# Kernel optimization log

Hardware: AMD Instinct MI355X
Metric: run time of the kernel (lower is better)

Reference implementation:

```python
import jax, jax.numpy as jnp
import numpy as np

B, S, D, E, TOPK, H = 8, 2048, 2048, 8, 2, 16
DH = D // H          # head_dim = 128
FH = D // H          # head_hidden_dim = 128 (hidden == dim, forced by linear3 shapes)
ROUTE_LEN = 2048     # x0 = x[:, :2048]


def setup_inputs() -> dict:
    key = jax.random.key(0)
    ks = jax.random.split(key, 8)
    s = 0.02
    return {
        "x": jax.random.normal(ks[0], (B, S, D), jnp.float32),
        "switch_w": jax.random.normal(ks[1], (E, D * ROUTE_LEN), jnp.float32) * s,
        "switch_b": jnp.zeros((E,), jnp.float32),
        "w1": jax.random.normal(ks[2], (E, FH, DH), jnp.float32) * s,
        "b1": jnp.zeros((E, FH), jnp.float32),
        "w2": jax.random.normal(ks[3], (E, DH, FH), jnp.float32) * s,
        "b2": jnp.zeros((E, DH), jnp.float32),
        "w3": jax.random.normal(ks[4], (D, D), jnp.float32) * s,
        "b3": jnp.zeros((D,), jnp.float32),
    }


def reference(x, switch_w, switch_b, w1, b1, w2, b2, w3, b3):
    b, s, d = x.shape
    # --- router: per batch-sample softmax over experts, top-k selection ---
    x0 = x[:, :ROUTE_LEN].reshape(b, -1)                      # [B, 2048*D]
    logits = x0 @ switch_w.T + switch_b                       # [B, E]
    probs = jax.nn.softmax(logits, axis=-1)
    gate, top_idx = jax.lax.top_k(probs, TOPK)                # [B, K]
    # --- split heads ---
    xh = x.reshape(b, s, H, DH).transpose(0, 2, 1, 3)         # [B, H, S, Dh]
    # --- per-sample gather of selected expert weights (dense grouped GEMM) ---
    w1s, b1s = w1[top_idx], b1[top_idx]                       # [B,K,F,Dh], [B,K,F]
    w2s, b2s = w2[top_idx], b2[top_idx]                       # [B,K,Dh,F], [B,K,Dh]
    h = jnp.einsum('bhsd,bkfd->bkhsf', xh, w1s) + b1s[:, :, None, None, :]
    h = jax.nn.gelu(h, approximate=False)                     # torch nn.GELU is exact
    o = jnp.einsum('bkhsf,bkdf->bkhsd', h, w2s) + b2s[:, :, None, None, :]
    # gate-weighted combine over selected experts (index_add_ sums the k copies)
    o = (o * gate[:, :, None, None, None]).sum(axis=1)        # [B, H, S, Dh]
    o = o.transpose(0, 2, 1, 3).reshape(b, s, d)              # combine heads
    out = x + o                                               # residual
    return out @ w3.T + b3                                    # linear3
```

## Files before the change

kernel.cpp:

```cpp
#include <hip/hip_runtime.h>
#include <math.h>

typedef unsigned short u16;
typedef unsigned int u32;
typedef __attribute__((ext_vector_type(8))) short short8;
typedef __attribute__((ext_vector_type(4))) float f32x4;
typedef __attribute__((ext_vector_type(4))) unsigned short ushort4v;

#define B_ 8
#define S_ 2048
#define D_ 2048
#define H_ 16
#define RLEN 4194304
#define NCHUNK 512

static __device__ __forceinline__ u16 f2bf(float f) {
    union { float f; u32 u; } v; v.f = f;
    u32 r = v.u + 0x7fffu + ((v.u >> 16) & 1u);
    return (u16)(r >> 16);
}
static __device__ __forceinline__ float bf2f(u16 u) {
    union { u32 u; float f; } v; v.u = ((u32)u) << 16;
    return v.f;
}
static __device__ __forceinline__ float gelu_fast(float v) {
    float z = 1.5957691216057308f * v * (1.0f + 0.044715f * v * v);
    float e = __expf(z);
    float r = __builtin_amdgcn_rcpf(e + 1.0f);
    return v * (1.0f - r);
}
static __device__ __forceinline__ f32x4 ntload4(const float* p) {
    return __builtin_nontemporal_load((const f32x4*)p);
}

typedef const __attribute__((address_space(1))) u32* gas1_t;
typedef __attribute__((address_space(3))) u32* las3_t;
static __device__ __forceinline__ void gload_lds16(const void* g, void* l) {
    __builtin_amdgcn_global_load_lds((gas1_t)g, (las3_t)l, 16, 0, 0);
}

template<int XB>
__global__ __launch_bounds__(256, 3) void router_partial(const float* __restrict__ x,
                                                         const float* __restrict__ sw,
                                                         float* __restrict__ part,
                                                         u16* __restrict__ xb) {
    int c = blockIdx.x;
    int t = threadIdx.x;
    const int chunk = RLEN / NCHUNK;
    int base = c * chunk;
    float acc[8][8];
#pragma unroll
    for (int b = 0; b < 8; b++)
#pragma unroll
        for (int e = 0; e < 8; e++) acc[b][e] = 0.f;

    for (int it = 0; it < chunk / (256 * 4); ++it) {
        int i = base + (it * 256 + t) * 4;
        f32x4 xv[8];
#pragma unroll
        for (int b = 0; b < 8; b++) xv[b] = ntload4(&x[(size_t)b * RLEN + i]);
        if (XB) {
            int row = i >> 7, col = i & 127;
            int scol = (((col >> 3) ^ (row & 7)) << 3) | (col & 7);
#pragma unroll
            for (int b = 0; b < 8; b++) {
                ushort4v u;
                u.x = f2bf(xv[b].x); u.y = f2bf(xv[b].y);
                u.z = f2bf(xv[b].z); u.w = f2bf(xv[b].w);
                *(ushort4v*)&xb[(size_t)b * RLEN + (size_t)row * 128 + scol] = u;
            }
        }
        f32x4 sv = ntload4(&sw[i]);
#pragma unroll
        for (int e = 0; e < 8; e++) {
            f32x4 svn;
            if (e < 7) svn = ntload4(&sw[(size_t)(e + 1) * RLEN + i]);
#pragma unroll
            for (int b = 0; b < 8; b++)
                acc[b][e] += xv[b].x * sv.x + xv[b].y * sv.y +
                             xv[b].z * sv.z + xv[b].w * sv.w;
            sv = svn;
        }
    }

    __shared__ float red[4][64];
    int lane = t & 63, wv = t >> 6;
#pragma unroll
    for (int q = 0; q < 64; q++) {
        float v = acc[q >> 3][q & 7];
#pragma unroll
        for (int m = 32; m >= 1; m >>= 1) v += __shfl_xor(v, m, 64);
        if (lane == 0) red[wv][q] = v;
    }
    __syncthreads();
    if (t < 64) {
        float s = red[0][t] + red[1][t] + red[2][t] + red[3][t];
        part[(size_t)t * NCHUNK + c] = s;
    }
}

__global__ __launch_bounds__(512) void router_finish(const float* __restrict__ part,
                                                     const float* __restrict__ swb,
                                                     const float* __restrict__ b2,
                                                     float* __restrict__ gate,
                                                     int* __restrict__ idx,
                                                     float* __restrict__ bc) {
    int t = threadIdx.x;
    __shared__ float lg[64];
    __shared__ float sg[16];
    __shared__ int   si[16];
    {
        int row = t >> 3, seg = t & 7;
        const float* p = part + (size_t)row * NCHUNK + seg * 64;
        float s = 0.f;
#pragma unroll 8
        for (int c = 0; c < 64; c++) s += p[c];
#pragma unroll
        for (int m = 4; m >= 1; m >>= 1) s += __shfl_down(s, m, 64);
        if (seg == 0) lg[row] = s + swb[row & 7];
    }
    __syncthreads();
    if (t < 8) {
        int b = t;
        float m = -1e30f;
        for (int e = 0; e < 8; e++) m = fmaxf(m, lg[b * 8 + e]);
        float p[8]; float sum = 0.f;
        for (int e = 0; e < 8; e++) { p[e] = expf(lg[b * 8 + e] - m); sum += p[e]; }
        for (int e = 0; e < 8; e++) p[e] /= sum;
        int i1 = 0; float v1 = p[0];
        for (int e = 1; e < 8; e++) if (p[e] > v1) { v1 = p[e]; i1 = e; }
        int i2 = -1; float v2 = -1.f;
        for (int e = 0; e < 8; e++) if (e != i1 && p[e] > v2) { v2 = p[e]; i2 = e; }
        gate[b * 2 + 0] = v1; gate[b * 2 + 1] = v2;
        idx[b * 2 + 0] = i1;  idx[b * 2 + 1] = i2;
        sg[b * 2] = v1; sg[b * 2 + 1] = v2;
        si[b * 2] = i1; si[b * 2 + 1] = i2;
    }
    __syncthreads();
    if (t < 128)
        for (int b = 0; b < 8; b++)
            bc[b * 128 + t] = sg[b * 2] * b2[si[b * 2] * 128 + t] +
                              sg[b * 2 + 1] * b2[si[b * 2 + 1] * 128 + t];
}

__global__ __launch_bounds__(256) void convert_w12(const float* __restrict__ w1,
                                                   const float* __restrict__ w2,
                                                   u16* __restrict__ w1b,
                                                   u16* __restrict__ w2b) {
    int i4 = (blockIdx.x * 256 + threadIdx.x) * 4;
    if (i4 < 131072) {
        int k = i4 & 127, f = (i4 >> 7) & 127;
        float4 v = *(const float4*)&w1[i4];
        int sc = ((((k >> 3) ^ (f & 7)) << 3) | (k & 7));
        ushort4v u;
        u.x = f2bf(v.x); u.y = f2bf(v.y); u.z = f2bf(v.z); u.w = f2bf(v.w);
        *(ushort4v*)&w1b[(i4 & ~127) + sc] = u;
    } else {
        int j = i4 - 131072;
        float4 v = *(const float4*)&w2[j];
        ushort4v u;
        u.x = f2bf(v.x); u.y = f2bf(v.y); u.z = f2bf(v.z); u.w = f2bf(v.w);
        *(ushort4v*)&w2b[j] = u;
    }
}

__global__ __launch_bounds__(256) void convert_w3(const float* __restrict__ w3,
                                                  u16* __restrict__ w3b) {
    size_t i = ((size_t)blockIdx.x * 256 + threadIdx.x) * 4;
    float4 v = *(const float4*)&w3[i];
    u16* d = &w3b[i];
    d[0] = f2bf(v.x); d[1] = f2bf(v.y); d[2] = f2bf(v.z); d[3] = f2bf(v.w);
}

template<int XB>
__global__ __launch_bounds__(512) void mlp_kernel(const void* __restrict__ xsrc_,
                                                  const u16* __restrict__ w1b,
                                                  const u16* __restrict__ w2b,
                                                  const float* __restrict__ b1,
                                                  const float* __restrict__ gate,
                                                  const int* __restrict__ idx,
                                                  const float* __restrict__ bc,
                                                  u16* __restrict__ y) {
    __shared__ __align__(16) u16 w1s[256 * 128];
    __shared__ __align__(16) u16 xs[2][64 * 128];
    __shared__ __align__(16) u16 hb[2][32 * 256];
    __shared__ __align__(16) u16 ob[2][32 * 128];
    const int t = threadIdx.x, lane = t & 63, w = t >> 6;
    const int wr = w >> 2, wq = w & 3;
    const int l15 = lane & 15, l4 = lane >> 4;
    const int b = blockIdx.y, grp = blockIdx.x;
    const size_t xbase = (size_t)b * RLEN;
    const size_t gbase = xbase + (size_t)grp * 65536;
    const int e0 = idx[b * 2], e1 = idx[b * 2 + 1];
    const int slot = wq >> 1;
    const float gw = gate[b * 2 + slot];
    const float* b1p = b1 + (slot ? e1 : e0) * 128;

    float b1v[4];
#pragma unroll
    for (int nt = 0; nt < 4; nt++) b1v[nt] = b1p[(wq & 1) * 64 + nt * 16 + l15];
    float bcv[2];
#pragma unroll
    for (int n = 0; n < 2; n++) bcv[n] = bc[b * 128 + wq * 32 + n * 16 + l15];

    short8 w2f[2][8];
#pragma unroll
    for (int n = 0; n < 2; n++) {
        int d = wq * 32 + n * 16 + l15;
#pragma unroll
        for (int kb = 0; kb < 8; kb++) {
            int e = (kb >= 4) ? e1 : e0;
            int f = (kb & 3) * 32 + l4 * 8;
            w2f[n][kb] = *(const short8*)&w2b[((size_t)(e * 128 + d)) * 128 + f];
        }
    }

#pragma unroll
    for (int p = 0; p < 8; p++) {
        int elem = p * 4096 + t * 8;
        int frow = elem >> 7, col = elem & 127;
        int e = (frow >= 128) ? e1 : e0;
        gload_lds16(w1b + ((size_t)(e * 128 + (frow & 127))) * 128 + col,
                    (char*)w1s + elem * 2);
    }
    if (XB) {
        const u16* xbp = (const u16*)xsrc_;
#pragma unroll
        for (int T = 0; T < 2; T++) {
            gload_lds16(xbp + gbase + T * 8192 + t * 8, (char*)&xs[T][0] + t * 16);
            gload_lds16(xbp + gbase + T * 8192 + 4096 + t * 8,
                        (char*)&xs[T][0] + 8192 + t * 16);
        }
        asm volatile("s_waitcnt vmcnt(0)" ::: "memory");
    } else {
        const float* xf = (const float*)xsrc_;
#pragma unroll
        for (int T = 0; T < 2; T++)
#pragma unroll
            for (int p = 0; p < 4; p++) {
                int elem = p * 2048 + t * 4;
                int row = elem >> 7, col = elem & 127;
                float4 v = *(const float4*)&xf[gbase + T * 8192 + elem];
                ushort4v u;
                u.x = f2bf(v.x); u.y = f2bf(v.y); u.z = f2bf(v.z); u.w = f2bf(v.w);
                *(ushort4v*)((char*)&xs[T][0] + row * 256 +
                             (((col >> 3) ^ (row & 7)) << 4) + (col & 7) * 2) = u;
            }
        asm volatile("s_waitcnt vmcnt(0) lgkmcnt(0)" ::: "memory");
    }
    __builtin_amdgcn_s_barrier();

    auto G1 = [&](int st, f32x4* a1) {
        const u16* xc = &xs[(st >> 1) & 1][0];
        int rbase = (st & 1) * 32 + wr * 16 + l15;
#pragma unroll
        for (int nt = 0; nt < 4; nt++) a1[nt] = (f32x4){0.f, 0.f, 0.f, 0.f};
#pragma unroll
        for (int kb = 0; kb < 4; kb++) {
            int kg = kb * 4 + l4;
            short8 a = *(const short8*)&xc[rbase * 128 + ((kg ^ (rbase & 7)) << 3)];
#pragma unroll
            for (int nt = 0; nt < 4; nt++) {
                int fr = wq * 64 + nt * 16 + l15;
                short8 bb = *(const short8*)&w1s[fr * 128 + ((kg ^ (fr & 7)) << 3)];
                a1[nt] = __builtin_amdgcn_mfma_f32_16x16x32_bf16(a, bb, a1[nt], 0, 0, 0);
            }
        }
    };
    auto GELU_ST = [&](int st, f32x4* a1) {
        u16* hd = &hb[st & 1][0];
#pragma unroll
        for (int nt = 0; nt < 4; nt++) {
            int fcol = wq * 64 + nt * 16 + l15;
#pragma unroll
            for (int j = 0; j < 4; j++) {
                int row = wr * 16 + l4 * 4 + j;
                float v = a1[nt][j] + b1v[nt];
                v = gelu_fast(v) * gw;
                hd[row * 256 + ((((fcol >> 3) ^ (row & 7)) << 3) | (fcol & 7))] = f2bf(v);
            }
        }
    };
    auto G2 = [&](int st, f32x4* a2) {
        const u16* hs = &hb[st & 1][0];
        int arow = wr * 16 + l15;
        a2[0] = (f32x4){0.f, 0.f, 0.f, 0.f};
        a2[1] = (f32x4){0.f, 0.f, 0.f, 0.f};
#pragma unroll
        for (int kb = 0; kb < 8; kb++) {
            int fg = kb * 4 + l4;
            short8 a = *(const short8*)&hs[arow * 256 + ((fg ^ (arow & 7)) << 3)];
            a2[0] = __builtin_amdgcn_mfma_f32_16x16x32_bf16(a, w2f[0][kb], a2[0], 0, 0, 0);
            a2[1] = __builtin_amdgcn_mfma_f32_16x16x32_bf16(a, w2f[1][kb], a2[1], 0, 0, 0);
        }
    };
    auto OWRITE = [&](int st, f32x4* a2) {
        u16* od = &ob[st & 1][0];
        const u16* xc = &xs[(st >> 1) & 1][0];
#pragma unroll
        for (int n = 0; n < 2; n++) {
            int d = wq * 32 + n * 16 + l15;
#pragma unroll
            for (int j = 0; j < 4; j++) {
                int row = wr * 16 + l4 * 4 + j;
                int xrow = (st & 1) * 32 + row;
                float xr = bf2f(xc[xrow * 128 + ((((d >> 3) ^ (xrow & 7)) << 3) | (d & 7))]);
                od[row * 128 + (d ^ ((row & 7) << 3))] = f2bf(a2[n][j] + bcv[n] + xr);
            }
        }
    };
    auto YSTV = [&](int st) {
        int row = t >> 4;
        int cg = t & 15;
        const u16* os = &ob[st & 1][0];
        short8 v = *(const short8*)&os[row * 128 + ((cg ^ (row & 7)) << 3)];
        u16* yb = y + xbase + (size_t)grp * 65536 + st * 4096;
        *(short8*)&yb[row * 128 + cg * 8] = v;
    };

    {
        f32x4 a1[4];
        G1(0, a1);
        GELU_ST(0, a1);
    }
    asm volatile("s_waitcnt lgkmcnt(0)" ::: "memory");
    __builtin_amdgcn_s_barrier();

    for (int st = 0; st < 17; ++st) {
        const bool stg = (st < 16) && ((st & 1) == 0) && st >= 2 && st <= 12;
        if (st < 16) {
            f32x4 a1n[4];
            if (st < 15) G1(st + 1, a1n);
            f32x4 a2[2];
            G2(st, a2);
            if (st < 15) GELU_ST(st + 1, a1n);
            OWRITE(st, a2);
        }
        if (stg) {
            int T = st / 2 + 1;
            if (XB) {
                const u16* xbp = (const u16*)xsrc_;
                gload_lds16(xbp + gbase + T * 8192 + t * 8, (char*)&xs[T & 1][0] + t * 16);
                gload_lds16(xbp + gbase + T * 8192 + 4096 + t * 8,
                            (char*)&xs[T & 1][0] + 8192 + t * 16);
            } else {
                const float* xf = (const float*)xsrc_;
#pragma unroll
                for (int p = 0; p < 4; p++) {
                    int elem = p * 2048 + t * 4;
                    int row = elem >> 7, col = elem & 127;
                    float4 v = *(const float4*)&xf[gbase + T * 8192 + elem];
                    ushort4v u;
                    u.x = f2bf(v.x); u.y = f2bf(v.y); u.z = f2bf(v.z); u.w = f2bf(v.w);
                    *(ushort4v*)((char*)&xs[T & 1][0] + row * 256 +
                                 (((col >> 3) ^ (row & 7)) << 4) + (col & 7) * 2) = u;
                }
            }
        }
        if (st >= 1) YSTV(st - 1);
        asm volatile("s_waitcnt lgkmcnt(0)" ::: "memory");
        if (stg && XB) asm volatile("s_waitcnt vmcnt(1)" ::: "memory");
        if (st < 16) __builtin_amdgcn_s_barrier();
    }
}

#define BARX() do { asm volatile("" ::: "memory"); __builtin_amdgcn_s_barrier(); \
                    asm volatile("" ::: "memory"); } while (0)

#define WLG(NSTR) do { asm volatile("s_waitcnt lgkmcnt(" NSTR ")" ::: "memory"); \
                       __builtin_amdgcn_sched_barrier(0); } while (0)

#define DSA(mh, c) do { \
    const char* _ba = smem + (c) * 65536 + abase; \
    _Pragma("unroll") for (int mf = 0; mf < 4; mf++) \
    _Pragma("unroll") for (int kk = 0; kk < 2; kk++) \
        areg[mf][kk] = *(const short8*)(_ba + ((mh) * 4 + mf) * 2048 + kof[kk]); \
} while (0)

#define DSB(nh, c) do { \
    const char* _bb = smem + (c) * 65536 + bbase; \
    _Pragma("unroll") for (int nf = 0; nf < 2; nf++) \
    _Pragma("unroll") for (int kk = 0; kk < 2; kk++) \
        breg[(nh) * 2 + nf][kk] = *(const short8*)(_bb + ((nh) * 2 + nf) * 2048 + kof[kk]); \
} while (0)

#define MMAQ(mh, nh) do { \
    __builtin_amdgcn_s_setprio(1); \
    _Pragma("unroll") for (int mf = 0; mf < 4; mf++) \
    _Pragma("unroll") for (int nf = 0; nf < 2; nf++) \
    _Pragma("unroll") for (int kk = 0; kk < 2; kk++) \
        acc[(mh) * 4 + mf][(nh) * 2 + nf] = __builtin_amdgcn_mfma_f32_16x16x32_bf16( \
            areg[mf][kk], breg[(nh) * 2 + nf][kk], acc[(mh) * 4 + mf][(nh) * 2 + nf], 0, 0, 0); \
    __builtin_amdgcn_s_setprio(0); \
} while (0)

#define STG(op, c, h, kt) do { \
    const u16* _gs = (op) ? wbp : yap; \
    int _tr0 = (op) ? nrow0 : mrow0; \
    _Pragma("unroll") for (int p = 0; p < 2; p++) { \
        int _idx = p * 512 + t; \
        int _row = _idx >> 3; \
        int _gcol = (((_idx & 7) ^ (_row & 7)) << 3); \
        gload_lds16(_gs + (size_t)(_tr0 + (h) * 128 + _row) * 2048 + (kt) * 64 + _gcol, \
                    smem + (c) * 65536 + (op) * 32768 + (h) * 16384 + _idx * 16); \
    } \
} while (0)

__global__ __launch_bounds__(512, 2) void final_gemm256(const u16* __restrict__ yap,
                                                        const u16* __restrict__ wbp,
                                                        const float* __restrict__ b3,
                                                        float* __restrict__ out) {
    extern __shared__ char smem[];
    const int t = threadIdx.x;
    const int lane = t & 63, w = t >> 6;
    const int wm = w >> 2, wn = w & 3;
    const int l15 = lane & 15, l4 = lane >> 4, sx = lane & 7;

    int bid = blockIdx.x;
    int xcd = bid & 7, q = bid >> 3;
    const int mrow0 = (xcd * 8 + (q >> 3)) * 256;
    const int nrow0 = (q & 7) * 256;

    const int abase = wm * 16384 + l15 * 128;
    const int bbase = 32768 + (wn >> 1) * 16384 + ((wn & 1) * 64 + l15) * 128;
    int kof[2];
#pragma unroll
    for (int kk = 0; kk < 2; kk++) kof[kk] = ((kk * 4 + l4) ^ sx) << 4;

    f32x4 acc[8][4];
#pragma unroll
    for (int m = 0; m < 8; m++)
#pragma unroll
        for (int n = 0; n < 4; n++) acc[m][n] = (f32x4){0.f, 0.f, 0.f, 0.f};
    short8 areg[4][2];
    short8 breg[4][2];

    STG(0, 0, 0, 0); STG(0, 0, 1, 0); STG(1, 0, 0, 0); STG(1, 0, 1, 0);
    STG(0, 1, 0, 1); STG(0, 1, 1, 1); STG(1, 1, 0, 1); STG(1, 1, 1, 1);
    asm volatile("s_waitcnt vmcnt(8)" ::: "memory");
    BARX();
    DSA(0, 0); DSB(0, 0); DSB(1, 0);

    for (int it2 = 0; it2 < 16; ++it2) {
#pragma unroll
        for (int c = 0; c < 2; ++c) {
            const int tt = 2 * it2 + c;
            WLG("4");  MMAQ(0, 0);
            WLG("0");  MMAQ(0, 1);
            DSA(1, c);
            WLG("0");  MMAQ(1, 0);
            asm volatile("s_waitcnt vmcnt(0)" ::: "memory");
            BARX();
            if (tt < 30) { STG(0, c, 0, tt + 2); STG(0, c, 1, tt + 2);
                           STG(1, c, 0, tt + 2); STG(1, c, 1, tt + 2); }
            MMAQ(1, 1);
            if (tt < 31) { DSA(0, c ^ 1); DSB(0, c ^ 1); DSB(1, c ^ 1); }
        }
    }

#pragma unroll
    for (int m = 0; m < 8; m++)
#pragma unroll
        for (int n = 0; n < 4; n++) {
            int col = nrow0 + wn * 64 + n * 16 + l15;
            float bias = b3[col];
            int row = mrow0 + wm * 128 + m * 16 + l4 * 4;
#pragma unroll
            for (int j = 0; j < 4; j++)
                out[(size_t)(row + j) * 2048 + col] = acc[m][n][j] + bias;
        }
}

extern "C" void kernel_launch(void* const* d_in, const int* in_sizes, int n_in,
                              void* d_out, int out_size, void* d_ws, size_t ws_size,
                              hipStream_t stream) {
    const float* x   = (const float*)d_in[0];
    const float* sw  = (const float*)d_in[1];
    const float* swb = (const float*)d_in[2];
    const float* w1  = (const float*)d_in[3];
    const float* b1  = (const float*)d_in[4];
    const float* w2  = (const float*)d_in[5];
    const float* b2  = (const float*)d_in[6];
    const float* w3  = (const float*)d_in[7];
    const float* b3  = (const float*)d_in[8];
    float* out = (float*)d_out;

    char* ws = (char*)d_ws;
    float* part = (float*)(ws + 0);
    float* gate = (float*)(ws + 131072);
    int*   idx  = (int*)(ws + 131136);
    float* bc   = (float*)(ws + 131200);
    u16*   w1b  = (u16*)(ws + 262144);
    u16*   w2b  = (u16*)(ws + 524288);
    u16*   w3b  = (u16*)(ws + 786432);
    u16*   y    = (u16*)(ws + 9175040);
    u16*   xb   = (u16*)(ws + 76283904);
    const size_t need_xb = 143392768;
    const bool xbmode = ws_size >= need_xb;

    hipFuncSetAttribute((const void*)final_gemm256,
                        hipFuncAttributeMaxDynamicSharedMemorySize, 131072);

    if (xbmode)
        hipLaunchKernelGGL((router_partial<1>), dim3(NCHUNK), dim3(256), 0, stream, x, sw, part, xb);
    else
        hipLaunchKernelGGL((router_partial<0>), dim3(NCHUNK), dim3(256), 0, stream, x, sw, part, xb);
    hipLaunchKernelGGL(router_finish, dim3(1), dim3(512), 0, stream, part, swb, b2, gate, idx, bc);
    hipLaunchKernelGGL(convert_w12, dim3(256), dim3(256), 0, stream, w1, w2, w1b, w2b);
    hipLaunchKernelGGL(convert_w3, dim3(D_ * D_ / 1024), dim3(256), 0, stream, w3, w3b);
    if (xbmode)
        hipLaunchKernelGGL((mlp_kernel<1>), dim3(64, 8), dim3(512), 0, stream,
                           (const void*)xb, w1b, w2b, b1, gate, idx, bc, y);
    else
        hipLaunchKernelGGL((mlp_kernel<0>), dim3(64, 8), dim3(512), 0, stream,
                           (const void*)x, w1b, w2b, b1, gate, idx, bc, y);
    hipLaunchKernelGGL(final_gemm256, dim3(512), dim3(512), 131072, stream,
                       y, w3b, b3, out);
}
```

Measured before the change: 295.6 us.

## Keep W1 fragments in registers and double-buffer A fragments in final GEMM

Measured after the change: 377.6 us. 27.7% more time.

```diff
diff --git a/kernel.cpp b/kernel.cpp
--- a/kernel.cpp
+++ b/kernel.cpp
@@ -181,7 +181,6 @@
                                                   const int* __restrict__ idx,
                                                   const float* __restrict__ bc,
                                                   u16* __restrict__ y) {
-    __shared__ __align__(16) u16 w1s[256 * 128];
     __shared__ __align__(16) u16 xs[2][64 * 128];
     __shared__ __align__(16) u16 hb[2][32 * 256];
     __shared__ __align__(16) u16 ob[2][32 * 128];
@@ -193,8 +192,9 @@
     const size_t gbase = xbase + (size_t)grp * 65536;
     const int e0 = idx[b * 2], e1 = idx[b * 2 + 1];
     const int slot = wq >> 1;
+    const int esel = slot ? e1 : e0;
     const float gw = gate[b * 2 + slot];
-    const float* b1p = b1 + (slot ? e1 : e0) * 128;
+    const float* b1p = b1 + esel * 128;
 
     float b1v[4];
 #pragma unroll
@@ -203,6 +203,16 @@
 #pragma unroll
     for (int n = 0; n < 2; n++) bcv[n] = bc[b * 128 + wq * 32 + n * 16 + l15];
 
+    short8 w1f[4][4];
+#pragma unroll
+    for (int nt = 0; nt < 4; nt++)
+#pragma unroll
+        for (int kb = 0; kb < 4; kb++) {
+            int kg = kb * 4 + l4;
+            int fr = (wq & 1) * 64 + nt * 16 + l15;
+            w1f[nt][kb] = *(const short8*)&w1b[((size_t)(esel * 128 + fr)) * 128 +
+                                               ((kg ^ (l15 & 7)) << 3)];
+        }
     short8 w2f[2][8];
 #pragma unroll
     for (int n = 0; n < 2; n++) {
@@ -215,14 +225,6 @@
         }
     }
 
-#pragma unroll
-    for (int p = 0; p < 8; p++) {
-        int elem = p * 4096 + t * 8;
-        int frow = elem >> 7, col = elem & 127;
-        int e = (frow >= 128) ? e1 : e0;
-        gload_lds16(w1b + ((size_t)(e * 128 + (frow & 127))) * 128 + col,
-                    (char*)w1s + elem * 2);
-    }
     if (XB) {
         const u16* xbp = (const u16*)xsrc_;
 #pragma unroll
@@ -260,11 +262,8 @@
             int kg = kb * 4 + l4;
             short8 a = *(const short8*)&xc[rbase * 128 + ((kg ^ (rbase & 7)) << 3)];
 #pragma unroll
-            for (int nt = 0; nt < 4; nt++) {
-                int fr = wq * 64 + nt * 16 + l15;
-                short8 bb = *(const short8*)&w1s[fr * 128 + ((kg ^ (fr & 7)) << 3)];
-                a1[nt] = __builtin_amdgcn_mfma_f32_16x16x32_bf16(a, bb, a1[nt], 0, 0, 0);
-            }
+            for (int nt = 0; nt < 4; nt++)
+                a1[nt] = __builtin_amdgcn_mfma_f32_16x16x32_bf16(a, w1f[nt][kb], a1[nt], 0, 0, 0);
         }
     };
     auto GELU_ST = [&](int st, f32x4* a1) {
@@ -370,11 +369,11 @@
 #define WLG(NSTR) do { asm volatile("s_waitcnt lgkmcnt(" NSTR ")" ::: "memory"); \
                        __builtin_amdgcn_sched_barrier(0); } while (0)
 
-#define DSA(mh, c) do { \
+#define DSAx(dst, mh, c) do { \
     const char* _ba = smem + (c) * 65536 + abase; \
     _Pragma("unroll") for (int mf = 0; mf < 4; mf++) \
     _Pragma("unroll") for (int kk = 0; kk < 2; kk++) \
-        areg[mf][kk] = *(const short8*)(_ba + ((mh) * 4 + mf) * 2048 + kof[kk]); \
+        dst[mf][kk] = *(const short8*)(_ba + ((mh) * 4 + mf) * 2048 + kof[kk]); \
 } while (0)
 
 #define DSB(nh, c) do { \
@@ -384,13 +383,13 @@
         breg[(nh) * 2 + nf][kk] = *(const short8*)(_bb + ((nh) * 2 + nf) * 2048 + kof[kk]); \
 } while (0)
 
-#define MMAQ(mh, nh) do { \
+#define MMAQx(ar, mh, nh) do { \
     __builtin_amdgcn_s_setprio(1); \
     _Pragma("unroll") for (int mf = 0; mf < 4; mf++) \
     _Pragma("unroll") for (int nf = 0; nf < 2; nf++) \
     _Pragma("unroll") for (int kk = 0; kk < 2; kk++) \
         acc[(mh) * 4 + mf][(nh) * 2 + nf] = __builtin_amdgcn_mfma_f32_16x16x32_bf16( \
-            areg[mf][kk], breg[(nh) * 2 + nf][kk], acc[(mh) * 4 + mf][(nh) * 2 + nf], 0, 0, 0); \
+            ar[mf][kk], breg[(nh) * 2 + nf][kk], acc[(mh) * 4 + mf][(nh) * 2 + nf], 0, 0, 0); \
     __builtin_amdgcn_s_setprio(0); \
 } while (0)
 
@@ -406,7 +405,9 @@
     } \
 } while (0)
 
-__global__ __launch_bounds__(512, 2) void final_gemm256(const u16* __restrict__ yap,
+#define ISSUE24(c) do { DSAx(areg0, 0, c); DSB(0, c); DSB(1, c); DSAx(areg1, 1, c); } while (0)
+
+__global__ __launch_bounds__(512, 1) void final_gemm256(const u16* __restrict__ yap,
                                                         const u16* __restrict__ wbp,
                                                         const float* __restrict__ b3,
                                                         float* __restrict__ out) {
@@ -432,29 +433,28 @@
     for (int m = 0; m < 8; m++)
 #pragma unroll
         for (int n = 0; n < 4; n++) acc[m][n] = (f32x4){0.f, 0.f, 0.f, 0.f};
-    short8 areg[4][2];
+    short8 areg0[4][2], areg1[4][2];
     short8 breg[4][2];
 
     STG(0, 0, 0, 0); STG(0, 0, 1, 0); STG(1, 0, 0, 0); STG(1, 0, 1, 0);
     STG(0, 1, 0, 1); STG(0, 1, 1, 1); STG(1, 1, 0, 1); STG(1, 1, 1, 1);
     asm volatile("s_waitcnt vmcnt(8)" ::: "memory");
     BARX();
-    DSA(0, 0); DSB(0, 0); DSB(1, 0);
+    ISSUE24(0);
 
     for (int it2 = 0; it2 < 16; ++it2) {
 #pragma unroll
         for (int c = 0; c < 2; ++c) {
             const int tt = 2 * it2 + c;
-            WLG("4");  MMAQ(0, 0);
-            WLG("0");  MMAQ(0, 1);
-            DSA(1, c);
-            WLG("0");  MMAQ(1, 0);
+            WLG("12"); MMAQx(areg0, 0, 0);
+            WLG("8");  MMAQx(areg0, 0, 1);
+            WLG("0");  MMAQx(areg1, 1, 0);
             asm volatile("s_waitcnt vmcnt(0)" ::: "memory");
             BARX();
             if (tt < 30) { STG(0, c, 0, tt + 2); STG(0, c, 1, tt + 2);
                            STG(1, c, 0, tt + 2); STG(1, c, 1, tt + 2); }
-            MMAQ(1, 1);
-            if (tt < 31) { DSA(0, c ^ 1); DSB(0, c ^ 1); DSB(1, c ^ 1); }
+            MMAQx(areg1, 1, 1);
+            if (tt < 31) ISSUE24(c ^ 1);
         }
     }
 
```
